# Kernel optimization log

Measured on AMD Instinct MI355X. Metric: run time of the kernel, lower is better.

The kernel has to match this reference:

```python
import jax, jax.numpy as jnp
import numpy as np

N, E, F_DIM, H = 50000, 800000, 128, 4


def setup_inputs() -> dict:
    key = jax.random.key(0)
    ks = jax.random.split(key, 12)
    x = jax.random.normal(ks[0], (N, F_DIM), dtype=jnp.float32)
    edge_index = jax.random.randint(ks[1], (2, E), 0, N, dtype=jnp.int64)
    s = 1.0 / np.sqrt(F_DIM)
    return {
        "x": x,
        "edge_index": edge_index,
        "W_gat": jax.random.normal(ks[2], (F_DIM, H * F_DIM), dtype=jnp.float32) * s,
        "att_src": jax.random.normal(ks[3], (H, F_DIM), dtype=jnp.float32) * s,
        "att_dst": jax.random.normal(ks[4], (H, F_DIM), dtype=jnp.float32) * s,
        "bias_gat": jnp.zeros((H * F_DIM,), dtype=jnp.float32),
        "W_mha": jax.random.normal(ks[5], (H * F_DIM, F_DIM), dtype=jnp.float32) * s,
        "b_mha": jnp.zeros((F_DIM,), dtype=jnp.float32),
        "W1": jax.random.normal(ks[6], (F_DIM, F_DIM), dtype=jnp.float32) * s,
        "b1": jnp.zeros((F_DIM,), dtype=jnp.float32),
        "W2": jax.random.normal(ks[7], (F_DIM, F_DIM), dtype=jnp.float32) * s,
        "b2": jnp.zeros((F_DIM,), dtype=jnp.float32),
    }


def gat_conv(x, src, dst, W_gat, att_src, att_dst, bias_gat):
    n = x.shape[0]
    xp = (x @ W_gat).reshape(n, H, F_DIM)            # [N,H,F]
    a_src = jnp.einsum('nhf,hf->nh', xp, att_src)    # [N,H]
    a_dst = jnp.einsum('nhf,hf->nh', xp, att_dst)
    alpha = jax.nn.leaky_relu(a_src[src] + a_dst[dst], 0.2)  # [E,H]
    m = jax.ops.segment_max(alpha, dst, num_segments=n)      # segment softmax over dst
    e = jnp.exp(alpha - m[dst])
    denom = jax.ops.segment_sum(e, dst, num_segments=n)
    att = e / denom[dst]                              # [E,H]
    msg = xp[src] * att[:, :, None]                   # [E,H,F] gather-weight
    out = jax.ops.segment_sum(msg, dst, num_segments=n)  # [N,H,F]
    return out.reshape(n, H * F_DIM) + bias_gat


def reference(x, edge_index, W_gat, att_src, att_dst, bias_gat, W_mha, b_mha, W1, b1, W2, b2):
    n = x.shape[0]
    # PyG GATConv default add_self_loops=True
    ar = jnp.arange(n, dtype=edge_index.dtype)
    src = jnp.concatenate([edge_index[0], ar])
    dst = jnp.concatenate([edge_index[1], ar])
    residual = x
    h = jax.nn.leaky_relu(gat_conv(x, src, dst, W_gat, att_src, att_dst, bias_gat), 0.01)
    h = h @ W_mha + b_mha + residual
    # Ffn
    res2 = h
    h = jax.nn.leaky_relu(h @ W1 + b1, 0.01)
    h = h @ W2 + b2 + res2
    return h
```

## Files before the change

kernel.cpp:

```cpp
#include <hip/hip_runtime.h>

#define FD 128
#define NH 4
#define HF 512
#define CAP 64
#define CSTR 16

typedef __attribute__((ext_vector_type(8))) short short8;
typedef __attribute__((ext_vector_type(4))) float v4f;

__device__ __forceinline__ float lrelu(float x, float s) { return x > 0.f ? x : s * x; }

__device__ __forceinline__ unsigned short f2bf(float f) {
    unsigned int u = __float_as_uint(f);
    u += 0x7FFFu + ((u >> 16) & 1u);
    return (unsigned short)(u >> 16);
}
__device__ __forceinline__ unsigned int pack2(float a, float b) {
    return (unsigned)f2bf(a) | ((unsigned)f2bf(b) << 16);
}

__global__ __launch_bounds__(256) void k_prep(const float* __restrict__ x,
                                              unsigned short* __restrict__ xb,
                                              const float* __restrict__ Wg, unsigned short* __restrict__ WgT,
                                              const float* __restrict__ Wm, unsigned short* __restrict__ WmT,
                                              const float* __restrict__ W1, unsigned short* __restrict__ W1T,
                                              const float* __restrict__ W2, unsigned short* __restrict__ W2T,
                                              const float* __restrict__ att_s,
                                              const float* __restrict__ att_d,
                                              float* __restrict__ U, int n) {
    const int t = threadIdx.x;
    int b = blockIdx.x;
    const int nCast = (n * FD / 8 + 255) / 256;
    const int nT1 = (FD * HF / 4 + 255) / 256;
    const int nT3 = (FD * FD / 4 + 255) / 256;
    if (b < nCast) {
        int i = b * 256 + t;
        if (i < n * FD / 8) {
            const float4* x4 = reinterpret_cast<const float4*>(x);
            float4 v0 = x4[i * 2], v1 = x4[i * 2 + 1];
            uint4 o;
            o.x = pack2(v0.x, v0.y); o.y = pack2(v0.z, v0.w);
            o.z = pack2(v1.x, v1.y); o.w = pack2(v1.z, v1.w);
            reinterpret_cast<uint4*>(xb)[i] = o;
        }
        return;
    }
    b -= nCast;
    if (b < nT1) {
        int i4 = (b * 256 + t) * 4;
        if (i4 < FD * HF) {
            int nn = i4 >> 7, k = i4 & 127;
            uint2 o;
            o.x = pack2(Wg[(size_t)k * HF + nn], Wg[(size_t)(k + 1) * HF + nn]);
            o.y = pack2(Wg[(size_t)(k + 2) * HF + nn], Wg[(size_t)(k + 3) * HF + nn]);
            *reinterpret_cast<uint2*>(&WgT[i4]) = o;
        }
        return;
    }
    b -= nT1;
    if (b < nT1) {
        int i4 = (b * 256 + t) * 4;
        if (i4 < HF * FD) {
            int nn = i4 >> 9, k = i4 & 511;
            uint2 o;
            o.x = pack2(Wm[(size_t)k * FD + nn], Wm[(size_t)(k + 1) * FD + nn]);
            o.y = pack2(Wm[(size_t)(k + 2) * FD + nn], Wm[(size_t)(k + 3) * FD + nn]);
            *reinterpret_cast<uint2*>(&WmT[i4]) = o;
        }
        return;
    }
    b -= nT1;
    if (b < nT3) {
        int i4 = (b * 256 + t) * 4;
        if (i4 < FD * FD) {
            int nn = i4 >> 7, k = i4 & 127;
            uint2 o;
            o.x = pack2(W1[(size_t)k * FD + nn], W1[(size_t)(k + 1) * FD + nn]);
            o.y = pack2(W1[(size_t)(k + 2) * FD + nn], W1[(size_t)(k + 3) * FD + nn]);
            *reinterpret_cast<uint2*>(&W1T[i4]) = o;
        }
        return;
    }
    b -= nT3;
    if (b < nT3) {
        int i4 = (b * 256 + t) * 4;
        if (i4 < FD * FD) {
            int nn = i4 >> 7, k = i4 & 127;
            uint2 o;
            o.x = pack2(W2[(size_t)k * FD + nn], W2[(size_t)(k + 1) * FD + nn]);
            o.y = pack2(W2[(size_t)(k + 2) * FD + nn], W2[(size_t)(k + 3) * FD + nn]);
            *reinterpret_cast<uint2*>(&W2T[i4]) = o;
        }
        return;
    }
    b -= nT3;
    {
        int idx = b * 256 + t;
        if (idx < 1024) {
            int type = idx >> 9, h = (idx >> 7) & 3, k = idx & 127;
            const float* att = type ? att_d : att_s;
            const float* wrow = &Wg[(size_t)k * HF + h * FD];
            const float* arow = &att[h * FD];
            float s = 0.f;
#pragma unroll 4
            for (int j = 0; j < FD; ++j) s += wrow[j] * arow[j];
            U[idx] = s;
        }
    }
}

__global__ __launch_bounds__(256) void k_alog(const unsigned short* __restrict__ xb,
                                              const float* __restrict__ U,
                                              float* __restrict__ a_s,
                                              float* __restrict__ a_d, int n) {
    int idx = blockIdx.x * 256 + threadIdx.x;
    int node = idx >> 2, h = idx & 3;
    if (node >= n) return;
    const uint4* xr = reinterpret_cast<const uint4*>(&xb[(size_t)node * FD]);
    const float* us = &U[h * FD];
    const float* ud = &U[512 + h * FD];
    float ps = 0.f, pd = 0.f;
#pragma unroll 4
    for (int j = 0; j < 16; ++j) {
        uint4 u = xr[j];
        const unsigned w[4] = {u.x, u.y, u.z, u.w};
#pragma unroll
        for (int q = 0; q < 4; ++q) {
            float f0 = __uint_as_float(w[q] << 16);
            float f1 = __uint_as_float(w[q] & 0xffff0000u);
            int c = j * 8 + q * 2;
            ps += f0 * us[c] + f1 * us[c + 1];
            pd += f0 * ud[c] + f1 * ud[c + 1];
        }
    }
    a_s[node * NH + h] = ps;
    a_d[node * NH + h] = pd;
}

__global__ __launch_bounds__(256) void k_scatter(const int* __restrict__ es,
                                                 const int* __restrict__ ed,
                                                 const float* __restrict__ a_s,
                                                 const float* __restrict__ a_d,
                                                 int* __restrict__ cur,
                                                 uint4* __restrict__ edata,
                                                 int E, int n, int NPX) {
    const int r = blockIdx.x & 7;
    const int chunk = blockIdx.x >> 3;
    const int lo = r * NPX;
    const int hi = min(lo + NPX, n);
    int i = chunk * 256 + threadIdx.x;
    if (i >= E) return;
    int d = ed[i];
    if (d < lo || d >= hi) return;
    int s = es[i];
    const float4 as = *reinterpret_cast<const float4*>(&a_s[(size_t)s * NH]);
    const float4 ad = *reinterpret_cast<const float4*>(&a_d[(size_t)d * NH]);
    float w0 = __expf(lrelu(as.x + ad.x, 0.2f));
    float w1 = __expf(lrelu(as.y + ad.y, 0.2f));
    float w2 = __expf(lrelu(as.z + ad.z, 0.2f));
    float w3 = __expf(lrelu(as.w + ad.w, 0.2f));
    int pos = atomicAdd(&cur[(size_t)d * CSTR], 1);
    if (pos < CAP) {
        uint4 rr;
        rr.x = (unsigned)s;
        rr.y = pack2(w0, w1);
        rr.z = pack2(w2, w3);
        rr.w = 0u;
        edata[(size_t)d * CAP + pos] = rr;
    }
}

#define GATH(REC) (*reinterpret_cast<const unsigned*>(&xb[(size_t)(int)(REC).x * FD + 2 * l]))
#define ACCUM(REC, U) do {                                                     \
    float w0_ = __uint_as_float((REC).y << 16);                                \
    float w1_ = __uint_as_float((REC).y & 0xffff0000u);                        \
    float w2_ = __uint_as_float((REC).z << 16);                                \
    float w3_ = __uint_as_float((REC).z & 0xffff0000u);                        \
    float g0_ = __uint_as_float((U) << 16);                                    \
    float g1_ = __uint_as_float((U) & 0xffff0000u);                            \
    ax0 += g0_ * w0_; ay0 += g1_ * w0_; den0 += w0_;                           \
    ax1 += g0_ * w1_; ay1 += g1_ * w1_; den1 += w1_;                           \
    ax2 += g0_ * w2_; ay2 += g1_ * w2_; den2 += w2_;                           \
    ax3 += g0_ * w3_; ay3 += g1_ * w3_; den3 += w3_;                           \
} while (0)

__global__ __launch_bounds__(256, 8) void k_aggr2(const unsigned short* __restrict__ xb,
                                                  const float* __restrict__ a_s,
                                                  const float* __restrict__ a_d,
                                                  const int* __restrict__ cur,
                                                  const uint4* __restrict__ edata,
                                                  unsigned short* __restrict__ agg,
                                                  int n, int NPX) {
    const int wv = threadIdx.x >> 6, l = threadIdx.x & 63;
    const int r = blockIdx.x & 7, j = blockIdx.x >> 3;
    const int node = r * NPX + j * 4 + wv;
    const int hi = min(r * NPX + NPX, n);
    if (node >= hi) return;
    const int un = __builtin_amdgcn_readfirstlane(node);

    const float4 as4 = *reinterpret_cast<const float4*>(&a_s[(size_t)node * NH]);
    const float4 ad4 = *reinterpret_cast<const float4*>(&a_d[(size_t)node * NH]);
    const float wS0 = __expf(lrelu(as4.x + ad4.x, 0.2f));
    const float wS1 = __expf(lrelu(as4.y + ad4.y, 0.2f));
    const float wS2 = __expf(lrelu(as4.z + ad4.z, 0.2f));
    const float wS3 = __expf(lrelu(as4.w + ad4.w, 0.2f));

    float ax0, ay0, ax1, ay1, ax2, ay2, ax3, ay3;
    float den0 = wS0, den1 = wS1, den2 = wS2, den3 = wS3;
    {
        unsigned ux = *reinterpret_cast<const unsigned*>(&xb[(size_t)node * FD + 2 * l]);
        float f0 = __uint_as_float(ux << 16);
        float f1 = __uint_as_float(ux & 0xffff0000u);
        ax0 = f0 * wS0; ay0 = f1 * wS0;
        ax1 = f0 * wS1; ay1 = f1 * wS1;
        ax2 = f0 * wS2; ay2 = f1 * wS2;
        ax3 = f0 * wS3; ay3 = f1 * wS3;
    }

    const uint4* p = edata + (size_t)un * CAP;
    int dg = __builtin_amdgcn_readfirstlane(cur[(size_t)un * CSTR]);
    dg = min(dg, CAP);
    int e = 0;
    for (; e + 8 <= dg; e += 8) {
        uint4 r0 = p[e], r1 = p[e + 1], r2 = p[e + 2], r3 = p[e + 3];
        uint4 r4 = p[e + 4], r5 = p[e + 5], r6 = p[e + 6], r7 = p[e + 7];
        unsigned u0 = GATH(r0), u1 = GATH(r1), u2 = GATH(r2), u3 = GATH(r3);
        unsigned u4 = GATH(r4), u5 = GATH(r5), u6 = GATH(r6), u7 = GATH(r7);
        ACCUM(r0, u0); ACCUM(r1, u1); ACCUM(r2, u2); ACCUM(r3, u3);
        ACCUM(r4, u4); ACCUM(r5, u5); ACCUM(r6, u6); ACCUM(r7, u7);
    }
    if (e + 4 <= dg) {
        uint4 r0 = p[e], r1 = p[e + 1], r2 = p[e + 2], r3 = p[e + 3];
        unsigned u0 = GATH(r0), u1 = GATH(r1), u2 = GATH(r2), u3 = GATH(r3);
        ACCUM(r0, u0); ACCUM(r1, u1); ACCUM(r2, u2); ACCUM(r3, u3);
        e += 4;
    }
    if (e + 2 <= dg) {
        uint4 r0 = p[e], r1 = p[e + 1];
        unsigned u0 = GATH(r0), u1 = GATH(r1);
        ACCUM(r0, u0); ACCUM(r1, u1);
        e += 2;
    }
    if (e < dg) {
        uint4 r0 = p[e];
        unsigned u0 = GATH(r0);
        ACCUM(r0, u0);
    }

    const float i0 = 1.f / den0, i1 = 1.f / den1, i2 = 1.f / den2, i3 = 1.f / den3;
    unsigned* ag = reinterpret_cast<unsigned*>(&agg[(size_t)node * HF + 2 * l]);
    ag[0]   = pack2(ax0 * i0, ay0 * i0);
    ag[64]  = pack2(ax1 * i1, ay1 * i1);
    ag[128] = pack2(ax2 * i2, ay2 * i2);
    ag[192] = pack2(ax3 * i3, ay3 * i3);
}

#define PREFETCH8(BP, STRIDE) do {                                             \
    _Pragma("unroll")                                                          \
    for (int rnd = 0; rnd < 8; ++rnd) {                                        \
        int r_ = rnd * 16 + sr;                                                \
        R[rnd] = *reinterpret_cast<const short8*>(&(BP)[(size_t)r_ * (STRIDE) + sc]); \
    } } while (0)

#define COMMIT8() do {                                                         \
    __syncthreads();                                                           \
    _Pragma("unroll")                                                          \
    for (int rnd = 0; rnd < 8; ++rnd) {                                        \
        int r_ = rnd * 16 + sr;                                                \
        *reinterpret_cast<short8*>(&WL[r_][sc]) = R[rnd];                      \
    }                                                                          \
    __syncthreads(); } while (0)

#define LOAD_A(HH) do {                                                        \
    _Pragma("unroll")                                                          \
    for (int kk = 0; kk < 4; ++kk) {                                           \
        RA0[kk] = *reinterpret_cast<const short8*>(                            \
            &agg[(size_t)amr0 * HF + (HH) * FD + kk * 32 + kg]);               \
        RA1[kk] = *reinterpret_cast<const short8*>(                            \
            &agg[(size_t)amr1 * HF + (HH) * FD + kk * 32 + kg]);               \
    } } while (0)

__global__ __launch_bounds__(256, 2) void k_tail(const unsigned short* __restrict__ agg,
                                                 const unsigned short* __restrict__ WgT,
                                                 const float* __restrict__ biasg,
                                                 const unsigned short* __restrict__ WmT,
                                                 const float* __restrict__ bm,
                                                 const float* __restrict__ x,
                                                 const unsigned short* __restrict__ W1T,
                                                 const float* __restrict__ b1,
                                                 const unsigned short* __restrict__ W2T,
                                                 const float* __restrict__ b2,
                                                 float* __restrict__ out, int n) {
    __shared__ unsigned short WL[128][132];
    __shared__ unsigned short tS[128][132];
    const int tid = threadIdx.x;
    const int m0 = blockIdx.x * 128;
    const int wv = tid >> 6, l = tid & 63;
    const int rA = l & 15;
    const int kg = (l >> 4) * 8;
    const int mw = m0 + wv * 32;
    const int amr0 = min(mw + rA, n - 1);
    const int amr1 = min(mw + 16 + rA, n - 1);
    const int sr = tid >> 4, sc = (tid & 15) * 8;

    short8 R[8];
    short8 RA0[4], RA1[4];
    v4f hma[2][8];
#pragma unroll
    for (int g = 0; g < 2; ++g)
#pragma unroll
        for (int t = 0; t < 8; ++t) hma[g][t] = (v4f){0.f, 0.f, 0.f, 0.f};

    LOAD_A(0);
    PREFETCH8(WgT, FD);

#pragma unroll
    for (int h = 0; h < 4; ++h) {
        COMMIT8();
        PREFETCH8(WmT + h * FD, HF);
        v4f acc[2][8];
#pragma unroll
        for (int g = 0; g < 2; ++g)
#pragma unroll
            for (int t = 0; t < 8; ++t) acc[g][t] = (v4f){0.f, 0.f, 0.f, 0.f};
        __builtin_amdgcn_s_setprio(1);
#pragma unroll
        for (int kk = 0; kk < 4; ++kk) {
#pragma unroll
            for (int nt = 0; nt < 8; ++nt) {
                short8 b = *reinterpret_cast<const short8*>(&WL[nt * 16 + rA][kk * 32 + kg]);
                acc[0][nt] = __builtin_amdgcn_mfma_f32_16x16x32_bf16(RA0[kk], b, acc[0][nt], 0, 0, 0);
                acc[1][nt] = __builtin_amdgcn_mfma_f32_16x16x32_bf16(RA1[kk], b, acc[1][nt], 0, 0, 0);
            }
        }
        __builtin_amdgcn_s_setprio(0);
#pragma unroll
        for (int g = 0; g < 2; ++g)
#pragma unroll
            for (int nt = 0; nt < 8; ++nt) {
                const int col = nt * 16 + rA;
                const float bv = biasg[h * FD + col];
#pragma unroll
                for (int i = 0; i < 4; ++i)
                    tS[wv * 32 + g * 16 + (l >> 4) * 4 + i][col] =
                        f2bf(lrelu(acc[g][nt][i] + bv, 0.01f));
            }
        COMMIT8();
        PREFETCH8((h < 3 ? WgT + (h + 1) * FD * FD : W1T), FD);
        if (h < 3) LOAD_A(h + 1);
        __builtin_amdgcn_s_setprio(1);
#pragma unroll
        for (int kk = 0; kk < 4; ++kk) {
            short8 a0 = *reinterpret_cast<const short8*>(&tS[wv * 32 + rA][kk * 32 + kg]);
            short8 a1 = *reinterpret_cast<const short8*>(&tS[wv * 32 + 16 + rA][kk * 32 + kg]);
#pragma unroll
            for (int nt = 0; nt < 8; ++nt) {
                short8 b = *reinterpret_cast<const short8*>(&WL[nt * 16 + rA][kk * 32 + kg]);
                hma[0][nt] = __builtin_amdgcn_mfma_f32_16x16x32_bf16(a0, b, hma[0][nt], 0, 0, 0);
                hma[1][nt] = __builtin_amdgcn_mfma_f32_16x16x32_bf16(a1, b, hma[1][nt], 0, 0, 0);
            }
        }
        __builtin_amdgcn_s_setprio(0);
    }

#pragma unroll
    for (int g = 0; g < 2; ++g)
#pragma unroll
        for (int nt = 0; nt < 8; ++nt) {
            const int col = nt * 16 + rA;
            const float bv = bm[col];
#pragma unroll
            for (int i = 0; i < 4; ++i) {
                const int r = min(mw + g * 16 + (l >> 4) * 4 + i, n - 1);
                float v = hma[g][nt][i] + bv + x[(size_t)r * FD + col];
                hma[g][nt][i] = v;
                tS[wv * 32 + g * 16 + (l >> 4) * 4 + i][col] = f2bf(v);
            }
        }
    COMMIT8();
    PREFETCH8(W2T, FD);
    v4f acc[2][8];
#pragma unroll
    for (int g = 0; g < 2; ++g)
#pragma unroll
        for (int t = 0; t < 8; ++t) acc[g][t] = (v4f){0.f, 0.f, 0.f, 0.f};
    __builtin_amdgcn_s_setprio(1);
#pragma unroll
    for (int kk = 0; kk < 4; ++kk) {
        short8 a0 = *reinterpret_cast<const short8*>(&tS[wv * 32 + rA][kk * 32 + kg]);
        short8 a1 = *reinterpret_cast<const short8*>(&tS[wv * 32 + 16 + rA][kk * 32 + kg]);
#pragma unroll
        for (int nt = 0; nt < 8; ++nt) {
            short8 b = *reinterpret_cast<const short8*>(&WL[nt * 16 + rA][kk * 32 + kg]);
            acc[0][nt] = __builtin_amdgcn_mfma_f32_16x16x32_bf16(a0, b, acc[0][nt], 0, 0, 0);
            acc[1][nt] = __builtin_amdgcn_mfma_f32_16x16x32_bf16(a1, b, acc[1][nt], 0, 0, 0);
        }
    }
    __builtin_amdgcn_s_setprio(0);
#pragma unroll
    for (int g = 0; g < 2; ++g)
#pragma unroll
        for (int nt = 0; nt < 8; ++nt) {
            const int col = nt * 16 + rA;
            const float bv = b1[col];
#pragma unroll
            for (int i = 0; i < 4; ++i)
                tS[wv * 32 + g * 16 + (l >> 4) * 4 + i][col] =
                    f2bf(lrelu(acc[g][nt][i] + bv, 0.01f));
        }
    COMMIT8();
#pragma unroll
    for (int g = 0; g < 2; ++g)
#pragma unroll
        for (int t = 0; t < 8; ++t) acc[g][t] = (v4f){0.f, 0.f, 0.f, 0.f};
    __builtin_amdgcn_s_setprio(1);
#pragma unroll
    for (int kk = 0; kk < 4; ++kk) {
        short8 a0 = *reinterpret_cast<const short8*>(&tS[wv * 32 + rA][kk * 32 + kg]);
        short8 a1 = *reinterpret_cast<const short8*>(&tS[wv * 32 + 16 + rA][kk * 32 + kg]);
#pragma unroll
        for (int nt = 0; nt < 8; ++nt) {
            short8 b = *reinterpret_cast<const short8*>(&WL[nt * 16 + rA][kk * 32 + kg]);
            acc[0][nt] = __builtin_amdgcn_mfma_f32_16x16x32_bf16(a0, b, acc[0][nt], 0, 0, 0);
            acc[1][nt] = __builtin_amdgcn_mfma_f32_16x16x32_bf16(a1, b, acc[1][nt], 0, 0, 0);
        }
    }
    __builtin_amdgcn_s_setprio(0);
#pragma unroll
    for (int g = 0; g < 2; ++g)
#pragma unroll
        for (int nt = 0; nt < 8; ++nt) {
            const int col = nt * 16 + rA;
            const float bv = b2[col];
#pragma unroll
            for (int i = 0; i < 4; ++i) {
                const int r = mw + g * 16 + (l >> 4) * 4 + i;
                if (r < n)
                    out[(size_t)r * FD + col] = acc[g][nt][i] + bv + hma[g][nt][i];
            }
        }
}

extern "C" void kernel_launch(void* const* d_in, const int* in_sizes, int n_in,
                              void* d_out, int out_size, void* d_ws, size_t ws_size,
                              hipStream_t stream) {
    const float* x     = (const float*)d_in[0];
    const int*   ei    = (const int*)d_in[1];
    const float* Wg    = (const float*)d_in[2];
    const float* att_s = (const float*)d_in[3];
    const float* att_d = (const float*)d_in[4];
    const float* biasg = (const float*)d_in[5];
    const float* Wm    = (const float*)d_in[6];
    const float* bm    = (const float*)d_in[7];
    const float* W1    = (const float*)d_in[8];
    const float* b1    = (const float*)d_in[9];
    const float* W2    = (const float*)d_in[10];
    const float* b2    = (const float*)d_in[11];
    float* out = (float*)d_out;

    const int n = in_sizes[0] / FD;
    const int E = in_sizes[1] / 2;
    const int* esrc = ei;
    const int* edst = ei + E;

    char* w = (char*)d_ws;
    size_t o = 0;
    auto alloc = [&](size_t b) { void* p = w + o; o = (o + b + 255) & ~(size_t)255; return p; };
    unsigned short* x_b  = (unsigned short*)alloc((size_t)n * FD * 2);
    unsigned short* WgT  = (unsigned short*)alloc((size_t)FD * HF * 2);
    unsigned short* WmT  = (unsigned short*)alloc((size_t)HF * FD * 2);
    unsigned short* W1T  = (unsigned short*)alloc((size_t)FD * FD * 2);
    unsigned short* W2T  = (unsigned short*)alloc((size_t)FD * FD * 2);
    float*          U    = (float*)alloc(1024 * 4);
    unsigned short* aggb = (unsigned short*)alloc((size_t)n * HF * 2);
    float* a_s   = (float*)alloc((size_t)n * NH * 4);
    float* a_d   = (float*)alloc((size_t)n * NH * 4);
    int*   cur   = (int*)alloc((size_t)n * CSTR * 4);
    uint4* edata = (uint4*)alloc((size_t)n * CAP * 16);

    hipMemsetAsync(cur, 0, (size_t)n * CSTR * 4, stream);

    const int NPX = (n + 7) / 8;
    const int nCast = (n * FD / 8 + 255) / 256;
    const int nT1 = (FD * HF / 4 + 255) / 256;
    const int nT3 = (FD * FD / 4 + 255) / 256;
    k_prep<<<nCast + 2 * nT1 + 2 * nT3 + 4, 256, 0, stream>>>(
        x, x_b, Wg, WgT, Wm, WmT, W1, W1T, W2, W2T, att_s, att_d, U, n);

    k_alog<<<(n * 4 + 255) / 256, 256, 0, stream>>>(x_b, U, a_s, a_d, n);

    const int NB = (E + 255) / 256;
    k_scatter<<<8 * NB, 256, 0, stream>>>(esrc, edst, a_s, a_d, cur, edata, E, n, NPX);
    const int GPX = (NPX + 3) / 4;
    k_aggr2<<<8 * GPX, 256, 0, stream>>>(x_b, a_s, a_d, cur, edata, aggb, n, NPX);

    const int mb2 = (n + 127) / 128;
    k_tail<<<mb2, 256, 0, stream>>>(aggb, WgT, biasg, WmT, bm, x, W1T, b1, W2T, b2, out, n);
}
```

Before: 171.8 us.

## Factor edge exp weights into per-node exponentials and scatter only source indices

Each node's score now has exp(a), exp(0.2a) and the raw value precomputed in a 16-float record. Per-edge softmax weights become a product of a source factor and a destination factor, with the factor pair picked by the sign of the summed logits. The scatter pass therefore stores only the 4-byte source index instead of a 16-byte record with packed bf16 weights, which cuts scatter traffic and the edge-list reads in aggregation. In exchange, aggregation must fetch a 48-byte per-source record for every edge. The product of exponentials could also overflow where the single exp of a bounded sum would not.

After: 215.4 us. +25.4%, slower.

```diff
diff --git a/kernel.cpp b/kernel.cpp
--- a/kernel.cpp
+++ b/kernel.cpp
@@ -112,8 +112,8 @@
 
 __global__ __launch_bounds__(256) void k_alog(const unsigned short* __restrict__ xb,
                                               const float* __restrict__ U,
-                                              float* __restrict__ a_s,
-                                              float* __restrict__ a_d, int n) {
+                                              float* __restrict__ PS,
+                                              float* __restrict__ PD, int n) {
     int idx = blockIdx.x * 256 + threadIdx.x;
     int node = idx >> 2, h = idx & 3;
     if (node >= n) return;
@@ -134,16 +134,16 @@
             pd += f0 * ud[c] + f1 * ud[c + 1];
         }
     }
-    a_s[node * NH + h] = ps;
-    a_d[node * NH + h] = pd;
+    float* psl = PS + (size_t)node * 16;
+    float* pdl = PD + (size_t)node * 16;
+    psl[h] = ps;  psl[4 + h] = __expf(ps);  psl[8 + h] = __expf(0.2f * ps);
+    pdl[h] = pd;  pdl[4 + h] = __expf(pd);  pdl[8 + h] = __expf(0.2f * pd);
 }
 
 __global__ __launch_bounds__(256) void k_scatter(const int* __restrict__ es,
                                                  const int* __restrict__ ed,
-                                                 const float* __restrict__ a_s,
-                                                 const float* __restrict__ a_d,
                                                  int* __restrict__ cur,
-                                                 uint4* __restrict__ edata,
+                                                 int* __restrict__ ssort,
                                                  int E, int n, int NPX) {
     const int r = blockIdx.x & 7;
     const int chunk = blockIdx.x >> 3;
@@ -153,32 +153,19 @@
     if (i >= E) return;
     int d = ed[i];
     if (d < lo || d >= hi) return;
-    int s = es[i];
-    const float4 as = *reinterpret_cast<const float4*>(&a_s[(size_t)s * NH]);
-    const float4 ad = *reinterpret_cast<const float4*>(&a_d[(size_t)d * NH]);
-    float w0 = __expf(lrelu(as.x + ad.x, 0.2f));
-    float w1 = __expf(lrelu(as.y + ad.y, 0.2f));
-    float w2 = __expf(lrelu(as.z + ad.z, 0.2f));
-    float w3 = __expf(lrelu(as.w + ad.w, 0.2f));
     int pos = atomicAdd(&cur[(size_t)d * CSTR], 1);
-    if (pos < CAP) {
-        uint4 rr;
-        rr.x = (unsigned)s;
-        rr.y = pack2(w0, w1);
-        rr.z = pack2(w2, w3);
-        rr.w = 0u;
-        edata[(size_t)d * CAP + pos] = rr;
-    }
-}
-
-#define GATH(REC) (*reinterpret_cast<const unsigned*>(&xb[(size_t)(int)(REC).x * FD + 2 * l]))
-#define ACCUM(REC, U) do {                                                     \
-    float w0_ = __uint_as_float((REC).y << 16);                                \
-    float w1_ = __uint_as_float((REC).y & 0xffff0000u);                        \
-    float w2_ = __uint_as_float((REC).z << 16);                                \
-    float w3_ = __uint_as_float((REC).z & 0xffff0000u);                        \
-    float g0_ = __uint_as_float((U) << 16);                                    \
-    float g1_ = __uint_as_float((U) & 0xffff0000u);                            \
+    if (pos < CAP) ssort[(size_t)d * CAP + pos] = es[i];
+}
+
+#define GX(S) (*reinterpret_cast<const unsigned*>(&xb[(size_t)(S) * FD + 2 * l]))
+#define WACC(S, UU) do {                                                       \
+    const float* ps_ = PS + (size_t)(S) * 16;                                  \
+    float w0_ = (ps_[0] + ad0 > 0.f) ? ps_[4] * E1d0 : ps_[8] * E2d0;          \
+    float w1_ = (ps_[1] + ad1 > 0.f) ? ps_[5] * E1d1 : ps_[9] * E2d1;          \
+    float w2_ = (ps_[2] + ad2 > 0.f) ? ps_[6] * E1d2 : ps_[10] * E2d2;         \
+    float w3_ = (ps_[3] + ad3 > 0.f) ? ps_[7] * E1d3 : ps_[11] * E2d3;         \
+    float g0_ = __uint_as_float((UU) << 16);                                   \
+    float g1_ = __uint_as_float((UU) & 0xffff0000u);                           \
     ax0 += g0_ * w0_; ay0 += g1_ * w0_; den0 += w0_;                           \
     ax1 += g0_ * w1_; ay1 += g1_ * w1_; den1 += w1_;                           \
     ax2 += g0_ * w2_; ay2 += g1_ * w2_; den2 += w2_;                           \
@@ -186,10 +173,10 @@
 } while (0)
 
 __global__ __launch_bounds__(256, 8) void k_aggr2(const unsigned short* __restrict__ xb,
-                                                  const float* __restrict__ a_s,
-                                                  const float* __restrict__ a_d,
+                                                  const float* __restrict__ PS,
+                                                  const float* __restrict__ PD,
                                                   const int* __restrict__ cur,
-                                                  const uint4* __restrict__ edata,
+                                                  const int* __restrict__ ssort,
                                                   unsigned short* __restrict__ agg,
                                                   int n, int NPX) {
     const int wv = threadIdx.x >> 6, l = threadIdx.x & 63;
@@ -199,16 +186,20 @@
     if (node >= hi) return;
     const int un = __builtin_amdgcn_readfirstlane(node);
 
-    const float4 as4 = *reinterpret_cast<const float4*>(&a_s[(size_t)node * NH]);
-    const float4 ad4 = *reinterpret_cast<const float4*>(&a_d[(size_t)node * NH]);
-    const float wS0 = __expf(lrelu(as4.x + ad4.x, 0.2f));
-    const float wS1 = __expf(lrelu(as4.y + ad4.y, 0.2f));
-    const float wS2 = __expf(lrelu(as4.z + ad4.z, 0.2f));
-    const float wS3 = __expf(lrelu(as4.w + ad4.w, 0.2f));
+    const float* pdl = PD + (size_t)un * 16;
+    const float ad0 = pdl[0], ad1 = pdl[1], ad2 = pdl[2], ad3 = pdl[3];
+    const float E1d0 = pdl[4], E1d1 = pdl[5], E1d2 = pdl[6], E1d3 = pdl[7];
+    const float E2d0 = pdl[8], E2d1 = pdl[9], E2d2 = pdl[10], E2d3 = pdl[11];
 
     float ax0, ay0, ax1, ay1, ax2, ay2, ax3, ay3;
-    float den0 = wS0, den1 = wS1, den2 = wS2, den3 = wS3;
+    float den0, den1, den2, den3;
     {
+        const float* psn = PS + (size_t)un * 16;
+        float wS0 = (psn[0] + ad0 > 0.f) ? psn[4] * E1d0 : psn[8] * E2d0;
+        float wS1 = (psn[1] + ad1 > 0.f) ? psn[5] * E1d1 : psn[9] * E2d1;
+        float wS2 = (psn[2] + ad2 > 0.f) ? psn[6] * E1d2 : psn[10] * E2d2;
+        float wS3 = (psn[3] + ad3 > 0.f) ? psn[7] * E1d3 : psn[11] * E2d3;
+        den0 = wS0; den1 = wS1; den2 = wS2; den3 = wS3;
         unsigned ux = *reinterpret_cast<const unsigned*>(&xb[(size_t)node * FD + 2 * l]);
         float f0 = __uint_as_float(ux << 16);
         float f1 = __uint_as_float(ux & 0xffff0000u);
@@ -218,34 +209,25 @@
         ax3 = f0 * wS3; ay3 = f1 * wS3;
     }
 
-    const uint4* p = edata + (size_t)un * CAP;
+    const int* p = ssort + (size_t)un * CAP;
     int dg = __builtin_amdgcn_readfirstlane(cur[(size_t)un * CSTR]);
     dg = min(dg, CAP);
     int e = 0;
-    for (; e + 8 <= dg; e += 8) {
-        uint4 r0 = p[e], r1 = p[e + 1], r2 = p[e + 2], r3 = p[e + 3];
-        uint4 r4 = p[e + 4], r5 = p[e + 5], r6 = p[e + 6], r7 = p[e + 7];
-        unsigned u0 = GATH(r0), u1 = GATH(r1), u2 = GATH(r2), u3 = GATH(r3);
-        unsigned u4 = GATH(r4), u5 = GATH(r5), u6 = GATH(r6), u7 = GATH(r7);
-        ACCUM(r0, u0); ACCUM(r1, u1); ACCUM(r2, u2); ACCUM(r3, u3);
-        ACCUM(r4, u4); ACCUM(r5, u5); ACCUM(r6, u6); ACCUM(r7, u7);
-    }
-    if (e + 4 <= dg) {
-        uint4 r0 = p[e], r1 = p[e + 1], r2 = p[e + 2], r3 = p[e + 3];
-        unsigned u0 = GATH(r0), u1 = GATH(r1), u2 = GATH(r2), u3 = GATH(r3);
-        ACCUM(r0, u0); ACCUM(r1, u1); ACCUM(r2, u2); ACCUM(r3, u3);
-        e += 4;
+    for (; e + 4 <= dg; e += 4) {
+        int s0 = p[e], s1 = p[e + 1], s2 = p[e + 2], s3 = p[e + 3];
+        unsigned u0 = GX(s0), u1 = GX(s1), u2 = GX(s2), u3 = GX(s3);
+        WACC(s0, u0); WACC(s1, u1); WACC(s2, u2); WACC(s3, u3);
     }
     if (e + 2 <= dg) {
-        uint4 r0 = p[e], r1 = p[e + 1];
-        unsigned u0 = GATH(r0), u1 = GATH(r1);
-        ACCUM(r0, u0); ACCUM(r1, u1);
+        int s0 = p[e], s1 = p[e + 1];
+        unsigned u0 = GX(s0), u1 = GX(s1);
+        WACC(s0, u0); WACC(s1, u1);
         e += 2;
     }
     if (e < dg) {
-        uint4 r0 = p[e];
-        unsigned u0 = GATH(r0);
-        ACCUM(r0, u0);
+        int s0 = p[e];
+        unsigned u0 = GX(s0);
+        WACC(s0, u0);
     }
 
     const float i0 = 1.f / den0, i1 = 1.f / den1, i2 = 1.f / den2, i3 = 1.f / den3;
@@ -474,10 +456,10 @@
     unsigned short* W2T  = (unsigned short*)alloc((size_t)FD * FD * 2);
     float*          U    = (float*)alloc(1024 * 4);
     unsigned short* aggb = (unsigned short*)alloc((size_t)n * HF * 2);
-    float* a_s   = (float*)alloc((size_t)n * NH * 4);
-    float* a_d   = (float*)alloc((size_t)n * NH * 4);
+    float* PS    = (float*)alloc((size_t)n * 16 * 4);
+    float* PD    = (float*)alloc((size_t)n * 16 * 4);
     int*   cur   = (int*)alloc((size_t)n * CSTR * 4);
-    uint4* edata = (uint4*)alloc((size_t)n * CAP * 16);
+    int*   ssort = (int*)alloc((size_t)n * CAP * 4);
 
     hipMemsetAsync(cur, 0, (size_t)n * CSTR * 4, stream);
 
@@ -488,12 +470,12 @@
     k_prep<<<nCast + 2 * nT1 + 2 * nT3 + 4, 256, 0, stream>>>(
         x, x_b, Wg, WgT, Wm, WmT, W1, W1T, W2, W2T, att_s, att_d, U, n);
 
-    k_alog<<<(n * 4 + 255) / 256, 256, 0, stream>>>(x_b, U, a_s, a_d, n);
+    k_alog<<<(n * 4 + 255) / 256, 256, 0, stream>>>(x_b, U, PS, PD, n);
 
     const int NB = (E + 255) / 256;
-    k_scatter<<<8 * NB, 256, 0, stream>>>(esrc, edst, a_s, a_d, cur, edata, E, n, NPX);
+    k_scatter<<<8 * NB, 256, 0, stream>>>(esrc, edst, cur, ssort, E, n, NPX);
     const int GPX = (NPX + 3) / 4;
-    k_aggr2<<<8 * GPX, 256, 0, stream>>>(x_b, a_s, a_d, cur, edata, aggb, n, NPX);
+    k_aggr2<<<8 * GPX, 256, 0, stream>>>(x_b, PS, PD, cur, ssort, aggb, n, NPX);
 
     const int mb2 = (n + 127) / 128;
     k_tail<<<mb2, 256, 0, stream>>>(aggb, WgT, biasg, WmT, bm, x, W1T, b1, W2T, b2, out, n);
```
